# Kernel tuning notes

Hardware: AMD Instinct MI355X
Metric: run time of the kernel (lower is better)

The kernel has to match this reference:

```python
import jax, jax.numpy as jnp
import numpy as np

V, SMAX, D, L, H, F = 50257, 1024, 768, 12, 12, 3072
DH = D // H
SCALE = float(np.sqrt(DH))


def setup_inputs() -> dict:
    key = jax.random.key(0)
    ks = jax.random.split(key, 24)
    B, S = 2, 1024
    std = 0.02
    inp = {
        'input_ids': jax.random.randint(ks[0], (B, S), 0, V),
        'tok_emb': jax.random.normal(ks[1], (V, D), jnp.float32) * std,
        'pos_emb': jax.random.normal(ks[2], (SMAX, D), jnp.float32) * std,
        # stacked per-layer params (leading dim L)
        'Wq': jax.random.normal(ks[3], (L, D, D), jnp.float32) * std,
        'bq': jnp.zeros((L, D), jnp.float32),
        'Wk': jax.random.normal(ks[4], (L, D, D), jnp.float32) * std,
        'bk': jnp.zeros((L, D), jnp.float32),
        'Wv': jax.random.normal(ks[5], (L, D, D), jnp.float32) * std,
        'bv': jnp.zeros((L, D), jnp.float32),
        'Wo': jax.random.normal(ks[6], (L, D, D), jnp.float32) * std,
        'bo': jnp.zeros((L, D), jnp.float32),
        'ln1_g': jnp.ones((L, D), jnp.float32),
        'ln1_b': jnp.zeros((L, D), jnp.float32),
        'ln2_g': jnp.ones((L, D), jnp.float32),
        'ln2_b': jnp.zeros((L, D), jnp.float32),
        'W1': jax.random.normal(ks[7], (L, D, F), jnp.float32) * std,
        'b1': jnp.zeros((L, F), jnp.float32),
        'W2': jax.random.normal(ks[8], (L, F, D), jnp.float32) * std,
        'b2': jnp.zeros((L, D), jnp.float32),
        'lnf_g': jnp.ones((D,), jnp.float32),
        'lnf_b': jnp.zeros((D,), jnp.float32),
        'Whead': jax.random.normal(ks[9], (D, V), jnp.float32) * std,
    }
    return inp


def _layernorm(x, g, b, eps=1e-5):
    mu = jnp.mean(x, axis=-1, keepdims=True)
    var = jnp.var(x, axis=-1, keepdims=True)
    return (x - mu) * jax.lax.rsqrt(var + eps) * g + b


def _gpt_forward(input_ids, tok_emb, pos_emb, Wq, bq, Wk, bk, Wv, bv, Wo, bo,
                 ln1_g, ln1_b, ln2_g, ln2_b, W1, b1, W2, b2, lnf_g, lnf_b, Whead):
    B, S = input_ids.shape
    x = tok_emb[input_ids] + pos_emb[:S][None, :, :]  # (B,S,D)
    # additive causal mask: -inf above the diagonal
    idx = jnp.arange(S)
    neg_inf = jnp.finfo(x.dtype).min
    mask = jnp.where(idx[None, :] > idx[:, None], neg_inf, 0.0).astype(x.dtype)  # (S,S)

    def block(x, p):
        (wq, bq_, wk, bk_, wv, bv_, wo, bo_, g1, b1_, g2, b2_, w1, bb1, w2, bb2) = p
        h = _layernorm(x, g1, b1_)
        q = (h @ wq + bq_).reshape(B, S, H, DH)
        k = (h @ wk + bk_).reshape(B, S, H, DH)
        v = (h @ wv + bv_).reshape(B, S, H, DH)
        scores = jnp.einsum('bqhd,bkhd->bhqk', q, k) / SCALE + mask
        attn = jax.nn.softmax(scores, axis=-1)
        o = jnp.einsum('bhqk,bkhd->bqhd', attn, v).reshape(B, S, D)
        x = x + (o @ wo + bo_)
        h2 = _layernorm(x, g2, b2_)
        ffn = jax.nn.gelu(h2 @ w1 + bb1, approximate=False) @ w2 + bb2
        return x + ffn, None

    params = (Wq, bq, Wk, bk, Wv, bv, Wo, bo, ln1_g, ln1_b, ln2_g, ln2_b, W1, b1, W2, b2)
    x, _ = jax.lax.scan(block, x, params)
    x = _layernorm(x, lnf_g, lnf_b)
    return x @ Whead  # (B,S,V) logits


def reference(input_ids, tok_emb, pos_emb, Wq, bq, Wk, bk, Wv, bv, Wo, bo,
              ln1_g, ln1_b, ln2_g, ln2_b, W1, b1, W2, b2, lnf_g, lnf_b, Whead):
    return _gpt_forward(input_ids, tok_emb, pos_emb, Wq, bq, Wk, bk, Wv, bv, Wo, bo,
                        ln1_g, ln1_b, ln2_g, ln2_b, W1, b1, W2, b2, lnf_g, lnf_b, Whead)
```

## Files before the change

### kernel.cpp

```cpp
#include <hip/hip_runtime.h>
#include <hip/hip_bf16.h>
#include <cstdint>
#include <cstddef>

#define DEV __device__ __forceinline__

typedef __attribute__((ext_vector_type(8))) short short8;
typedef __attribute__((ext_vector_type(4))) short s16x4;
typedef __attribute__((ext_vector_type(4))) float f32x4;
typedef unsigned short u16;
typedef unsigned int u32;

static constexpr int Vv = 50257;
static constexpr int Dd = 768;
static constexpr int Ll = 12;
static constexpr int Hh = 12;
static constexpr int Ff = 3072;
static constexpr int Ss = 1024;
static constexpr int Bbatch = 2;
static constexpr int DHh = 64;
static constexpr int Mtok = Bbatch * Ss;
static constexpr int NQKV = 3 * Dd;
static constexpr int VPAD = 50304;

DEV u16 f2bf(float f){ u32 x; __builtin_memcpy(&x, &f, 4); x += 0x7fffu + ((x >> 16) & 1u); return (u16)(x >> 16); }

DEV void gld_lds16(const void* g, void* l){
  __builtin_amdgcn_global_load_lds((const __attribute__((address_space(1))) void*)g,
                                   (__attribute__((address_space(3))) void*)l, 16, 0, 0);
}

template<int N> DEV void waitv(){
  if constexpr (N == 0) asm volatile("s_waitcnt vmcnt(0)" ::: "memory");
  else if constexpr (N == 2) asm volatile("s_waitcnt vmcnt(2)" ::: "memory");
  else if constexpr (N == 3) asm volatile("s_waitcnt vmcnt(3)" ::: "memory");
  else if constexpr (N == 4) asm volatile("s_waitcnt vmcnt(4)" ::: "memory");
}
DEV void barrier_sb(){
  __builtin_amdgcn_s_barrier();
  __builtin_amdgcn_sched_barrier(0);
}

__global__ void k_embed(const int* __restrict__ ids, const float* __restrict__ tok,
                        const float* __restrict__ pos, float* __restrict__ x){
  int t = blockIdx.x;
  int id = ids[t];
  int s = t & (Ss - 1);
  const float* tr = tok + (size_t)id * Dd;
  const float* pr = pos + (size_t)s * Dd;
  float* xr = x + (size_t)t * Dd;
  for (int c = threadIdx.x; c < Dd; c += blockDim.x) xr[c] = tr[c] + pr[c];
}

__global__ __launch_bounds__(256) void k_ln(const float* __restrict__ x, const float* __restrict__ g,
                                            const float* __restrict__ b, u16* __restrict__ y){
  int row = blockIdx.x, tid = threadIdx.x;
  const float* xr = x + (size_t)row * Dd;
  float v0 = xr[tid], v1 = xr[tid + 256], v2 = xr[tid + 512];
  float s = v0 + v1 + v2, ss = v0 * v0 + v1 * v1 + v2 * v2;
  for (int o = 1; o < 64; o <<= 1){ s += __shfl_xor(s, o, 64); ss += __shfl_xor(ss, o, 64); }
  __shared__ float red[8];
  int w = tid >> 6, l = tid & 63;
  if (l == 0){ red[w] = s; red[w + 4] = ss; }
  __syncthreads();
  s = red[0] + red[1] + red[2] + red[3];
  ss = red[4] + red[5] + red[6] + red[7];
  float mu = s * (1.0f / Dd);
  float var = ss * (1.0f / Dd) - mu * mu;
  float rs = rsqrtf(var + 1e-5f);
  u16* yr = y + (size_t)row * Dd;
  yr[tid]       = f2bf((v0 - mu) * rs * g[tid]       + b[tid]);
  yr[tid + 256] = f2bf((v1 - mu) * rs * g[tid + 256] + b[tid + 256]);
  yr[tid + 512] = f2bf((v2 - mu) * rs * g[tid + 512] + b[tid + 512]);
}

__global__ __launch_bounds__(256) void k_transpose(const float* __restrict__ src, u16* __restrict__ dst,
                                                   int R, int C, long smat, long dmat){
  __shared__ float tile[64][33];
  src += (size_t)blockIdx.z * smat;
  dst += (size_t)blockIdx.z * dmat;
  int c0 = blockIdx.x * 32, r0 = blockIdx.y * 64;
  int tid = threadIdx.x;
  int tc = tid & 31, tr = tid >> 5;
  #pragma unroll
  for (int i = 0; i < 8; i++){
    int r = tr + i * 8, c = c0 + tc;
    tile[r][tc] = (c < C) ? src[(size_t)(r0 + r) * C + c] : 0.0f;
  }
  __syncthreads();
  #pragma unroll
  for (int it = 0; it < 2; it++){
    int id = it * 256 + tid;
    int c = id & 31, rg = id >> 5, r = rg * 4;
    int cc = c0 + c;
    if (cc < C){
      s16x4 v = { (short)f2bf(tile[r][c]), (short)f2bf(tile[r + 1][c]),
                  (short)f2bf(tile[r + 2][c]), (short)f2bf(tile[r + 3][c]) };
      *(s16x4*)(dst + (size_t)cc * R + r0 + r) = v;
    }
  }
}

__global__ void k_biaspack(const float* __restrict__ bq, const float* __restrict__ bk,
                           const float* __restrict__ bv, float* __restrict__ o){
  int i = blockIdx.x * 256 + threadIdx.x;
  int col = i % NQKV, lay = i / NQKV;
  float v = (col < Dd) ? bq[lay * Dd + col]
          : (col < 2 * Dd) ? bk[lay * Dd + col - Dd]
          : bv[lay * Dd + col - 2 * Dd];
  o[i] = v;
}

__global__ __launch_bounds__(256) void k_combine(const float* __restrict__ p,
                                                 const float* __restrict__ bias,
                                                 float* __restrict__ x){
  int i = blockIdx.x * 256 + threadIdx.x;
  constexpr size_t SL = (size_t)Mtok * Dd;
  f32x4 a  = ((const f32x4*)x)[i];
  f32x4 q0 = ((const f32x4*)p)[i];
  f32x4 q1 = ((const f32x4*)(p + SL))[i];
  f32x4 q2 = ((const f32x4*)(p + 2 * SL))[i];
  f32x4 q3 = ((const f32x4*)(p + 3 * SL))[i];
  int col0 = (i * 4) % Dd;
  f32x4 bv = *(const f32x4*)(bias + col0);
  ((f32x4*)x)[i] = a + (q0 + q1) + (q2 + q3) + bv;
}

template<int BM, int BN, int STRIDE, int EPI>
__global__ __launch_bounds__(256) void k_gemm3(const u16* __restrict__ A, const u16* __restrict__ Bt,
    const float* __restrict__ bias, float* __restrict__ Cf, u16* __restrict__ Cb,
    u16* __restrict__ vt, int Nn, int MT, int NT){
  constexpr int HM = BM / 2, HN = BN / 2, FM = HM / 16, FN = HN / 16;
  constexpr int nA = (BM * 4) / 256, nB = (BN * 4) / 256, NL = nA + nB;
  constexpr int ABUF = BM * 32, BBUF = BN * 32;
  __shared__ __align__(16) u16 ldsA[3 * ABUF];
  __shared__ __align__(16) u16 ldsB[3 * BBUF];
  int tid = threadIdx.x, wid = tid >> 6, l = tid & 63;
  int wm = wid >> 1, wn = wid & 1;
  int lr = l & 15, lc = l >> 4;
  int nwg = gridDim.x, dIdx = blockIdx.x;
  int L = (dIdx & 7) * (nwg >> 3) + (dIdx >> 3);
  int kidx = 0;
  if (EPI == 4){ int per = MT * NT; kidx = L / per; L -= kidx * per; }
  int mtile = L % MT, ntile = L / MT;
  int m0 = mtile * BM, n0 = ntile * BN;
  int kbase = kidx * 768;

  const u16* gA[nA]; u16* dA[nA];
  const u16* gB[nB]; u16* dB[nB];
  #pragma unroll
  for (int i = 0; i < nA; i++){
    int id = i * 256 + tid, row = id >> 2, c = id & 3;
    int cs = c ^ ((row >> 1) & 3);
    gA[i] = A + (size_t)(m0 + row) * STRIDE + kbase + cs * 8;
    dA[i] = ldsA + id * 8;
  }
  #pragma unroll
  for (int i = 0; i < nB; i++){
    int id = i * 256 + tid, row = id >> 2, c = id & 3;
    int cs = c ^ ((row >> 1) & 3);
    gB[i] = Bt + (size_t)(n0 + row) * STRIDE + kbase + cs * 8;
    dB[i] = ldsB + id * 8;
  }
  int offA[FM], offB[FN];
  #pragma unroll
  for (int i = 0; i < FM; i++){
    int row = wm * HM + i * 16 + lr;
    offA[i] = row * 64 + ((lc ^ ((row >> 1) & 3)) << 4);
  }
  #pragma unroll
  for (int j = 0; j < FN; j++){
    int row = wn * HN + j * 16 + lr;
    offB[j] = row * 64 + ((lc ^ ((row >> 1) & 3)) << 4);
  }

  f32x4 acc[FM][FN];
  #pragma unroll
  for (int i = 0; i < FM; i++)
    #pragma unroll
    for (int j = 0; j < FN; j++) acc[i][j] = (f32x4)0.0f;

  auto stage = [&](int buf){
    #pragma unroll
    for (int i = 0; i < nA; i++){ gld_lds16(gA[i], dA[i] + buf * ABUF); gA[i] += 32; }
    #pragma unroll
    for (int i = 0; i < nB; i++){ gld_lds16(gB[i], dB[i] + buf * BBUF); gB[i] += 32; }
  };
  auto compute = [&](int buf){
    const char* bA = (const char*)(ldsA + buf * ABUF);
    const char* bB = (const char*)(ldsB + buf * BBUF);
    short8 af[FM], bfr[FN];
    #pragma unroll
    for (int i = 0; i < FM; i++) af[i] = *(const short8*)(bA + offA[i]);
    #pragma unroll
    for (int j = 0; j < FN; j++) bfr[j] = *(const short8*)(bB + offB[j]);
    __builtin_amdgcn_s_setprio(1);
    #pragma unroll
    for (int i = 0; i < FM; i++)
      #pragma unroll
      for (int j = 0; j < FN; j++)
        acc[i][j] = __builtin_amdgcn_mfma_f32_16x16x32_bf16(af[i], bfr[j], acc[i][j], 0, 0, 0);
    __builtin_amdgcn_s_setprio(0);
  };

  stage(0); stage(1);
  waitv<NL>(); barrier_sb();
  #pragma unroll 1
  for (int tt = 0; tt < 21; tt += 3){
    stage(2); compute(0); waitv<NL>(); barrier_sb();
    stage(0); compute(1); waitv<NL>(); barrier_sb();
    stage(1); compute(2); waitv<NL>(); barrier_sb();
  }
  stage(2); compute(0); waitv<NL>(); barrier_sb();
  compute(1); waitv<0>(); barrier_sb();
  compute(2);

  if (EPI == 4){
    float* P = Cf + (size_t)kidx * Mtok * Dd;
    #pragma unroll
    for (int i = 0; i < FM; i++)
      #pragma unroll
      for (int j = 0; j < FN; j++){
        int col = n0 + wn * HN + j * 16 + lr;
        #pragma unroll
        for (int r = 0; r < 4; r++){
          int row = m0 + wm * HM + i * 16 + lc * 4 + r;
          P[(size_t)row * Dd + col] = acc[i][j][r];
        }
      }
    return;
  }
  #pragma unroll
  for (int i = 0; i < FM; i++){
    #pragma unroll
    for (int j = 0; j < FN; j++){
      int col = n0 + wn * HN + j * 16 + lr;
      if (EPI == 0 && col >= Nn) continue;
      float bv = (EPI == 1 || EPI == 2 || EPI == 3) ? bias[col] : 0.0f;
      u16 q4[4];
      #pragma unroll
      for (int r = 0; r < 4; r++){
        int row = m0 + wm * HM + i * 16 + lc * 4 + r;
        float v = acc[i][j][r] + bv;
        if (EPI == 1){ if (col < Dd) v *= 0.125f; }
        if (EPI == 2) v = 0.5f * v * (1.0f + erff(v * 0.70710678118f));
        if (EPI == 0){
          Cf[(size_t)row * Nn + col] = v;
        } else if (EPI == 3){
          Cf[(size_t)row * Nn + col] += v;
        } else {
          u16 bvv = f2bf(v);
          q4[r] = bvv;
          Cb[(size_t)row * Nn + col] = bvv;
        }
      }
      if (EPI == 1 && col >= 2 * Dd){
        int c2 = col - 2 * Dd, hh = c2 >> 6, dd2 = c2 & 63;
        int rowb = m0 + wm * HM + i * 16 + lc * 4;
        int bb = rowb >> 10, ss2 = rowb & 1023;
        s16x4 v4 = { (short)q4[0], (short)q4[1], (short)q4[2], (short)q4[3] };
        *(s16x4*)(vt + (((size_t)((bb * Hh + hh) * DHh + dd2)) << 10) + ss2) = v4;
      }
    }
  }
}

__global__ __launch_bounds__(256) void k_attn(const u16* __restrict__ qkv, const u16* __restrict__ vt,
                                              u16* __restrict__ o){
  constexpr int KB = 64 * 64;
  __shared__ __align__(16) u16 ldsK[3 * KB];
  __shared__ __align__(16) u16 ldsV[3 * KB];
  __shared__ __align__(16) u16 ldsP[4][16 * 72];
  int iq = blockIdx.x, bh = blockIdx.y, b = bh / Hh, h = bh % Hh;
  int tid = threadIdx.x, wid = tid >> 6, l = tid & 63, lr = l & 15, lc = l >> 4;
  int nt = iq + 1;
  int qrow = b * Ss + iq * 64 + wid * 16 + lr;
  const u16* qp = qkv + (size_t)qrow * NQKV + h * DHh;
  short8 qf0 = *(const short8*)(qp + lc * 8);
  short8 qf1 = *(const short8*)(qp + 32 + lc * 8);

  const u16* gK[2]; const u16* gV[2]; u16* dK[2]; u16* dV[2];
  #pragma unroll
  for (int c = 0; c < 2; c++){
    int id = c * 256 + tid, row = id >> 3, ch = id & 7;
    int cs = ch ^ (row & 7);
    gK[c] = qkv + (size_t)(b * Ss + row) * NQKV + Dd + h * DHh + cs * 8;
    gV[c] = vt + ((size_t)(bh * DHh) + row) * Ss + cs * 8;
    dK[c] = ldsK + id * 8;
    dV[c] = ldsV + id * 8;
  }
  auto stage = [&](int soff){
    #pragma unroll
    for (int c = 0; c < 2; c++){ gld_lds16(gK[c], dK[c] + soff); gK[c] += (size_t)64 * NQKV; }
    #pragma unroll
    for (int c = 0; c < 2; c++){ gld_lds16(gV[c], dV[c] + soff); gV[c] += 64; }
  };
  int koff[4][2], voff[4][2];
  #pragma unroll
  for (int fn = 0; fn < 4; fn++){
    int kv = fn * 16 + lr;
    #pragma unroll
    for (int ks = 0; ks < 2; ks++){
      int ch = ks * 4 + lc;
      koff[fn][ks] = kv * 128 + ((ch ^ (kv & 7)) << 4);
      voff[fn][ks] = koff[fn][ks];
    }
  }

  float mreg[4], lsum[4];
  f32x4 oacc[4];
  #pragma unroll
  for (int r = 0; r < 4; r++){ mreg[r] = -1e30f; lsum[r] = 0.0f; }
  #pragma unroll
  for (int i = 0; i < 4; i++) oacc[i] = (f32x4)0.0f;
  u16* pbase = ldsP[wid];

  if (nt > 1){ stage(0); stage(KB); waitv<4>(); }
  else       { stage(0); waitv<0>(); }
  barrier_sb();

  int cb = 0;
  #pragma unroll 1
  for (int t = 0; t < nt; ++t){
    int sb = (cb >= KB) ? (cb - KB) : (cb + 2 * KB);
    if (t + 2 < nt) stage(sb);
    const char* kbse = (const char*)ldsK + cb * 2;
    const char* vbse = (const char*)ldsV + cb * 2;
    f32x4 sc[4];
    #pragma unroll
    for (int fn = 0; fn < 4; fn++) sc[fn] = (f32x4)0.0f;
    #pragma unroll
    for (int fn = 0; fn < 4; fn++){
      short8 kf0 = *(const short8*)(kbse + koff[fn][0]);
      short8 kf1 = *(const short8*)(kbse + koff[fn][1]);
      sc[fn] = __builtin_amdgcn_mfma_f32_16x16x32_bf16(qf0, kf0, sc[fn], 0, 0, 0);
      sc[fn] = __builtin_amdgcn_mfma_f32_16x16x32_bf16(qf1, kf1, sc[fn], 0, 0, 0);
    }
    if (t == iq){
      #pragma unroll
      for (int fn = 0; fn < 4; fn++){
        int kv = fn * 16 + lr;
        #pragma unroll
        for (int r = 0; r < 4; r++){
          int qr = wid * 16 + lc * 4 + r;
          if (kv > qr) sc[fn][r] = -1e30f;
        }
      }
    }
    float alpha[4];
    #pragma unroll
    for (int r = 0; r < 4; r++){
      float mx = fmaxf(fmaxf(sc[0][r], sc[1][r]), fmaxf(sc[2][r], sc[3][r]));
      mx = fmaxf(mx, __shfl_xor(mx, 1, 64));
      mx = fmaxf(mx, __shfl_xor(mx, 2, 64));
      mx = fmaxf(mx, __shfl_xor(mx, 4, 64));
      mx = fmaxf(mx, __shfl_xor(mx, 8, 64));
      float mnew = fmaxf(mreg[r], mx);
      alpha[r] = __expf(mreg[r] - mnew);
      mreg[r] = mnew;
      float rsum = 0.0f;
      #pragma unroll
      for (int fn = 0; fn < 4; fn++){
        float p = __expf(sc[fn][r] - mnew);
        sc[fn][r] = p;
        rsum += p;
      }
      rsum += __shfl_xor(rsum, 1, 64);
      rsum += __shfl_xor(rsum, 2, 64);
      rsum += __shfl_xor(rsum, 4, 64);
      rsum += __shfl_xor(rsum, 8, 64);
      lsum[r] = lsum[r] * alpha[r] + rsum;
    }
    #pragma unroll
    for (int fn = 0; fn < 4; fn++)
      #pragma unroll
      for (int r = 0; r < 4; r++)
        pbase[(lc * 4 + r) * 72 + fn * 16 + lr] = f2bf(sc[fn][r]);
    asm volatile("s_waitcnt lgkmcnt(0)" ::: "memory");
    __builtin_amdgcn_sched_barrier(0);
    #pragma unroll
    for (int fd = 0; fd < 4; fd++)
      #pragma unroll
      for (int r = 0; r < 4; r++) oacc[fd][r] *= alpha[r];
    short8 pa0 = *(const short8*)((const char*)pbase + lr * 144 + lc * 16);
    short8 pa1 = *(const short8*)((const char*)pbase + lr * 144 + (4 + lc) * 16);
    #pragma unroll
    for (int fd = 0; fd < 4; fd++){
      short8 vf0 = *(const short8*)(vbse + voff[fd][0]);
      short8 vf1 = *(const short8*)(vbse + voff[fd][1]);
      oacc[fd] = __builtin_amdgcn_mfma_f32_16x16x32_bf16(pa0, vf0, oacc[fd], 0, 0, 0);
      oacc[fd] = __builtin_amdgcn_mfma_f32_16x16x32_bf16(pa1, vf1, oacc[fd], 0, 0, 0);
    }
    if (t + 2 < nt) waitv<4>(); else waitv<0>();
    barrier_sb();
    cb = (cb == 2 * KB) ? 0 : (cb + KB);
  }
  #pragma unroll
  for (int fd = 0; fd < 4; fd++)
    #pragma unroll
    for (int r = 0; r < 4; r++){
      int row = b * Ss + iq * 64 + wid * 16 + lc * 4 + r;
      o[(size_t)row * Dd + h * DHh + fd * 16 + lr] = f2bf(oacc[fd][r] / lsum[r]);
    }
}

extern "C" void kernel_launch(void* const* d_in, const int* in_sizes, int n_in,
                              void* d_out, int out_size, void* d_ws, size_t ws_size,
                              hipStream_t stream){
  const int*   ids  = (const int*)d_in[0];
  const float* tok  = (const float*)d_in[1];
  const float* pos  = (const float*)d_in[2];
  const float* Wq   = (const float*)d_in[3];
  const float* bq   = (const float*)d_in[4];
  const float* Wk   = (const float*)d_in[5];
  const float* bk   = (const float*)d_in[6];
  const float* Wv   = (const float*)d_in[7];
  const float* bv   = (const float*)d_in[8];
  const float* Wo   = (const float*)d_in[9];
  const float* bo   = (const float*)d_in[10];
  const float* ln1g = (const float*)d_in[11];
  const float* ln1b = (const float*)d_in[12];
  const float* ln2g = (const float*)d_in[13];
  const float* ln2b = (const float*)d_in[14];
  const float* W1   = (const float*)d_in[15];
  const float* b1   = (const float*)d_in[16];
  const float* W2   = (const float*)d_in[17];
  const float* b2   = (const float*)d_in[18];
  const float* lnfg = (const float*)d_in[19];
  const float* lnfb = (const float*)d_in[20];
  const float* Wh   = (const float*)d_in[21];
  float* out = (float*)d_out;

  auto al = [](size_t x){ return (x + 255) & ~(size_t)255; };
  size_t off = 0;
  auto take = [&](size_t bytes){ size_t r = off; off = al(off + bytes); return r; };
  size_t o_x    = take((size_t)Mtok * Dd * 4);
  size_t o_h    = take((size_t)Mtok * Dd * 2);
  size_t o_qkv  = take((size_t)Mtok * NQKV * 2);
  size_t o_vt   = take((size_t)Bbatch * Hh * DHh * Ss * 2);
  size_t o_o    = take((size_t)Mtok * Dd * 2);
  size_t o_mid  = take((size_t)Mtok * Ff * 2);
  size_t o_bq   = take((size_t)Ll * NQKV * 4);
  size_t o_part = take((size_t)4 * Mtok * Dd * 4);
  size_t o_rot = off;
  size_t o_wqkv, o_wo, o_w1, o_w2, o_wh;
  bool full;
  {
    size_t t = off;
    o_wqkv = t; t = al(t + (size_t)Ll * NQKV * Dd * 2);
    o_wo   = t; t = al(t + (size_t)Ll * Dd * Dd * 2);
    o_w1   = t; t = al(t + (size_t)Ll * Ff * Dd * 2);
    o_w2   = t; t = al(t + (size_t)Ll * Dd * Ff * 2);
    o_wh   = t; t = al(t + (size_t)VPAD * Dd * 2);
    full = (t <= ws_size);
  }
  char* ws = (char*)d_ws;
  float* x    = (float*)(ws + o_x);
  u16*   h    = (u16*)(ws + o_h);
  u16*   qkvb = (u16*)(ws + o_qkv);
  u16*   vtb  = (u16*)(ws + o_vt);
  u16*   ob   = (u16*)(ws + o_o);
  u16*   midb = (u16*)(ws + o_mid);
  float* bqkvp= (float*)(ws + o_bq);
  float* part = (float*)(ws + o_part);
  u16* wqkvT = full ? (u16*)(ws + o_wqkv) : (u16*)(ws + o_rot);
  u16* woT   = full ? (u16*)(ws + o_wo)   : (u16*)(ws + o_rot);
  u16* w1T   = full ? (u16*)(ws + o_w1)   : (u16*)(ws + o_rot);
  u16* w2T   = full ? (u16*)(ws + o_w2)   : (u16*)(ws + o_rot);
  u16* whT   = full ? (u16*)(ws + o_wh)   : (u16*)(ws + o_rot);

  auto tpose = [&](const float* src, u16* dst, int R, int C, int nmat, long smat, long dmat){
    k_transpose<<<dim3((C + 31) / 32, R / 64, nmat), 256, 0, stream>>>(src, dst, R, C, smat, dmat);
  };

  k_biaspack<<<(Ll * NQKV) / 256, 256, 0, stream>>>(bq, bk, bv, bqkvp);
  k_embed<<<Mtok, 256, 0, stream>>>(ids, tok, pos, x);

  if (full){
    tpose(Wq, wqkvT,              Dd, Dd, Ll, (long)Dd * Dd, (long)NQKV * Dd);
    tpose(Wk, wqkvT + Dd * Dd,    Dd, Dd, Ll, (long)Dd * Dd, (long)NQKV * Dd);
    tpose(Wv, wqkvT + 2 * Dd * Dd,Dd, Dd, Ll, (long)Dd * Dd, (long)NQKV * Dd);
    tpose(Wo, woT, Dd, Dd, Ll, (long)Dd * Dd, (long)Dd * Dd);
    tpose(W1, w1T, Dd, Ff, Ll, (long)Dd * Ff, (long)Ff * Dd);
    tpose(W2, w2T, Ff, Dd, Ll, (long)Ff * Dd, (long)Dd * Ff);
    tpose(Wh, whT, Dd, Vv, 1, 0, 0);
  }

  auto gemm_qkv = [&](const u16* Aop, const u16* Bop, const float* bias, u16* Cb){
    constexpr int MT = Mtok / 64, NT = NQKV / 128;
    k_gemm3<64, 128, Dd, 1><<<MT * NT, 256, 0, stream>>>(Aop, Bop, bias, nullptr, Cb, vtb, NQKV, MT, NT);
  };
  auto gemm_wo = [&](const u16* Aop, const u16* Bop, const float* bias, float* C){
    constexpr int MT = Mtok / 64, NT = Dd / 64;
    k_gemm3<64, 64, Dd, 3><<<MT * NT, 256, 0, stream>>>(Aop, Bop, bias, C, nullptr, nullptr, Dd, MT, NT);
  };
  auto gemm_ffn1 = [&](const u16* Aop, const u16* Bop, const float* bias, u16* Cb){
    constexpr int MT = Mtok / 64, NT = Ff / 128;
    k_gemm3<64, 128, Dd, 2><<<MT * NT, 256, 0, stream>>>(Aop, Bop, bias, nullptr, Cb, nullptr, Ff, MT, NT);
  };
  auto gemm_ffn2 = [&](const u16* Aop, const u16* Bop){
    constexpr int MT = Mtok / 128, NT = Dd / 128;
    k_gemm3<128, 128, Ff, 4><<<MT * NT * 4, 256, 0, stream>>>(Aop, Bop, nullptr, part, nullptr, nullptr, Dd, MT, NT);
  };
  auto gemm_head = [&](const u16* Aop, const u16* Bop, float* C){
    constexpr int MT = Mtok / 128, NT = VPAD / 128;
    k_gemm3<128, 128, Dd, 0><<<MT * NT, 256, 0, stream>>>(Aop, Bop, nullptr, C, nullptr, nullptr, Vv, MT, NT);
  };

  for (int l = 0; l < Ll; ++l){
    const u16* wqkvL = full ? wqkvT + (size_t)l * NQKV * Dd : wqkvT;
    const u16* woL   = full ? woT   + (size_t)l * Dd * Dd   : woT;
    const u16* w1L   = full ? w1T   + (size_t)l * Ff * Dd   : w1T;
    const u16* w2L   = full ? w2T   + (size_t)l * Dd * Ff   : w2T;
    if (!full){
      tpose(Wq + (size_t)l * Dd * Dd, wqkvT,              Dd, Dd, 1, 0, 0);
      tpose(Wk + (size_t)l * Dd * Dd, wqkvT + Dd * Dd,    Dd, Dd, 1, 0, 0);
      tpose(Wv + (size_t)l * Dd * Dd, wqkvT + 2 * Dd * Dd,Dd, Dd, 1, 0, 0);
    }
    k_ln<<<Mtok, 256, 0, stream>>>(x, ln1g + l * Dd, ln1b + l * Dd, h);
    gemm_qkv(h, wqkvL, bqkvp + l * NQKV, qkvb);
    k_attn<<<dim3(Ss / 64, Bbatch * Hh), 256, 0, stream>>>(qkvb, vtb, ob);
    if (!full) tpose(Wo + (size_t)l * Dd * Dd, woT, Dd, Dd, 1, 0, 0);
    gemm_wo(ob, woL, bo + l * Dd, x);
    k_ln<<<Mtok, 256, 0, stream>>>(x, ln2g + l * Dd, ln2b + l * Dd, h);
    if (!full) tpose(W1 + (size_t)l * Dd * Ff, w1T, Dd, Ff, 1, 0, 0);
    gemm_ffn1(h, w1L, b1 + l * Ff, midb);
    if (!full) tpose(W2 + (size_t)l * Ff * Dd, w2T, Ff, Dd, 1, 0, 0);
    gemm_ffn2(midb, w2L);
    k_combine<<<(Mtok * Dd / 4) / 256, 256, 0, stream>>>(part, b2 + l * Dd, x);
  }
  k_ln<<<Mtok, 256, 0, stream>>>(x, lnfg, lnfb, h);
  if (!full) tpose(Wh, whT, Dd, Vv, 1, 0, 0);
  gemm_head(h, whT, out);
}
```

Baseline: 2.308 ms.

## Fuse layernorms into embed/combine, rework GEMM and attention kernels

```diff
diff --git a/kernel.cpp b/kernel.cpp
--- a/kernel.cpp
+++ b/kernel.cpp
@@ -30,26 +30,33 @@
                                    (__attribute__((address_space(3))) void*)l, 16, 0, 0);
 }
 
-template<int N> DEV void waitv(){
-  if constexpr (N == 0) asm volatile("s_waitcnt vmcnt(0)" ::: "memory");
-  else if constexpr (N == 2) asm volatile("s_waitcnt vmcnt(2)" ::: "memory");
-  else if constexpr (N == 3) asm volatile("s_waitcnt vmcnt(3)" ::: "memory");
-  else if constexpr (N == 4) asm volatile("s_waitcnt vmcnt(4)" ::: "memory");
-}
-DEV void barrier_sb(){
-  __builtin_amdgcn_s_barrier();
-  __builtin_amdgcn_sched_barrier(0);
-}
-
-__global__ void k_embed(const int* __restrict__ ids, const float* __restrict__ tok,
-                        const float* __restrict__ pos, float* __restrict__ x){
-  int t = blockIdx.x;
+__global__ __launch_bounds__(256) void k_embed_ln(const int* __restrict__ ids, const float* __restrict__ tok,
+                                                  const float* __restrict__ pos, const float* __restrict__ g,
+                                                  const float* __restrict__ b, float* __restrict__ x,
+                                                  u16* __restrict__ h){
+  int t = blockIdx.x, tid = threadIdx.x;
   int id = ids[t];
   int s = t & (Ss - 1);
   const float* tr = tok + (size_t)id * Dd;
   const float* pr = pos + (size_t)s * Dd;
+  float v0 = tr[tid] + pr[tid], v1 = tr[tid + 256] + pr[tid + 256], v2 = tr[tid + 512] + pr[tid + 512];
   float* xr = x + (size_t)t * Dd;
-  for (int c = threadIdx.x; c < Dd; c += blockDim.x) xr[c] = tr[c] + pr[c];
+  xr[tid] = v0; xr[tid + 256] = v1; xr[tid + 512] = v2;
+  float sm = v0 + v1 + v2, ss = v0 * v0 + v1 * v1 + v2 * v2;
+  for (int o = 1; o < 64; o <<= 1){ sm += __shfl_xor(sm, o, 64); ss += __shfl_xor(ss, o, 64); }
+  __shared__ float red[8];
+  int w = tid >> 6, l = tid & 63;
+  if (l == 0){ red[w] = sm; red[w + 4] = ss; }
+  __syncthreads();
+  sm = red[0] + red[1] + red[2] + red[3];
+  ss = red[4] + red[5] + red[6] + red[7];
+  float mu = sm * (1.0f / Dd);
+  float var = ss * (1.0f / Dd) - mu * mu;
+  float rs = rsqrtf(var + 1e-5f);
+  u16* yr = h + (size_t)t * Dd;
+  yr[tid]       = f2bf((v0 - mu) * rs * g[tid]       + b[tid]);
+  yr[tid + 256] = f2bf((v1 - mu) * rs * g[tid + 256] + b[tid + 256]);
+  yr[tid + 512] = f2bf((v2 - mu) * rs * g[tid + 512] + b[tid + 512]);
 }
 
 __global__ __launch_bounds__(256) void k_ln(const float* __restrict__ x, const float* __restrict__ g,
@@ -74,6 +81,35 @@
   yr[tid + 512] = f2bf((v2 - mu) * rs * g[tid + 512] + b[tid + 512]);
 }
 
+__global__ __launch_bounds__(256) void k_combineln(const float* __restrict__ p, const float* __restrict__ bias,
+                                                   float* __restrict__ x, const float* __restrict__ g,
+                                                   const float* __restrict__ b, u16* __restrict__ h){
+  constexpr size_t SL = (size_t)Mtok * Dd;
+  int row = blockIdx.x, tid = threadIdx.x;
+  float* xr = x + (size_t)row * Dd;
+  const float* p0 = p + (size_t)row * Dd;
+  const float* p1 = p0 + SL;
+  float v0 = xr[tid]       + p0[tid]       + p1[tid]       + bias[tid];
+  float v1 = xr[tid + 256] + p0[tid + 256] + p1[tid + 256] + bias[tid + 256];
+  float v2 = xr[tid + 512] + p0[tid + 512] + p1[tid + 512] + bias[tid + 512];
+  xr[tid] = v0; xr[tid + 256] = v1; xr[tid + 512] = v2;
+  float s = v0 + v1 + v2, ss = v0 * v0 + v1 * v1 + v2 * v2;
+  for (int o = 1; o < 64; o <<= 1){ s += __shfl_xor(s, o, 64); ss += __shfl_xor(ss, o, 64); }
+  __shared__ float red[8];
+  int w = tid >> 6, l = tid & 63;
+  if (l == 0){ red[w] = s; red[w + 4] = ss; }
+  __syncthreads();
+  s = red[0] + red[1] + red[2] + red[3];
+  ss = red[4] + red[5] + red[6] + red[7];
+  float mu = s * (1.0f / Dd);
+  float var = ss * (1.0f / Dd) - mu * mu;
+  float rs = rsqrtf(var + 1e-5f);
+  u16* yr = h + (size_t)row * Dd;
+  yr[tid]       = f2bf((v0 - mu) * rs * g[tid]       + b[tid]);
+  yr[tid + 256] = f2bf((v1 - mu) * rs * g[tid + 256] + b[tid + 256]);
+  yr[tid + 512] = f2bf((v2 - mu) * rs * g[tid + 512] + b[tid + 512]);
+}
+
 __global__ __launch_bounds__(256) void k_transpose(const float* __restrict__ src, u16* __restrict__ dst,
                                                    int R, int C, long smat, long dmat){
   __shared__ float tile[64][33];
@@ -111,40 +147,29 @@
   o[i] = v;
 }
 
-__global__ __launch_bounds__(256) void k_combine(const float* __restrict__ p,
-                                                 const float* __restrict__ bias,
-                                                 float* __restrict__ x){
-  int i = blockIdx.x * 256 + threadIdx.x;
-  constexpr size_t SL = (size_t)Mtok * Dd;
-  f32x4 a  = ((const f32x4*)x)[i];
-  f32x4 q0 = ((const f32x4*)p)[i];
-  f32x4 q1 = ((const f32x4*)(p + SL))[i];
-  f32x4 q2 = ((const f32x4*)(p + 2 * SL))[i];
-  f32x4 q3 = ((const f32x4*)(p + 3 * SL))[i];
-  int col0 = (i * 4) % Dd;
-  f32x4 bv = *(const f32x4*)(bias + col0);
-  ((f32x4*)x)[i] = a + (q0 + q1) + (q2 + q3) + bv;
-}
-
-template<int BM, int BN, int STRIDE, int EPI>
-__global__ __launch_bounds__(256) void k_gemm3(const u16* __restrict__ A, const u16* __restrict__ Bt,
+template<int BM, int BN, int EPI>
+__global__ __launch_bounds__(256) void k_gemmF(const u16* __restrict__ A, const u16* __restrict__ Bt,
     const float* __restrict__ bias, float* __restrict__ Cf, u16* __restrict__ Cb,
     u16* __restrict__ vt, int Nn, int MT, int NT){
+  constexpr bool SPLIT = (EPI == 4);
+  constexpr int KST  = SPLIT ? Ff : Dd;
+  constexpr int KLEN = SPLIT ? (Ff / 2) : Dd;
+  constexpr int nk = KLEN / 32;
   constexpr int HM = BM / 2, HN = BN / 2, FM = HM / 16, FN = HN / 16;
-  constexpr int nA = (BM * 4) / 256, nB = (BN * 4) / 256, NL = nA + nB;
-  constexpr int ABUF = BM * 32, BBUF = BN * 32;
-  __shared__ __align__(16) u16 ldsA[3 * ABUF];
-  __shared__ __align__(16) u16 ldsB[3 * BBUF];
+  constexpr int nA = (BM * 4) / 256, nB = (BN * 4) / 256;
+  constexpr int ABYTE = BM * 64, BBYTE = BN * 64;
+  __shared__ __align__(16) u16 ldsA[2 * BM * 32];
+  __shared__ __align__(16) u16 ldsB[2 * BN * 32];
   int tid = threadIdx.x, wid = tid >> 6, l = tid & 63;
   int wm = wid >> 1, wn = wid & 1;
   int lr = l & 15, lc = l >> 4;
   int nwg = gridDim.x, dIdx = blockIdx.x;
   int L = (dIdx & 7) * (nwg >> 3) + (dIdx >> 3);
   int kidx = 0;
-  if (EPI == 4){ int per = MT * NT; kidx = L / per; L -= kidx * per; }
+  if (SPLIT){ int per = MT * NT; kidx = L / per; L -= kidx * per; }
   int mtile = L % MT, ntile = L / MT;
   int m0 = mtile * BM, n0 = ntile * BN;
-  int kbase = kidx * 768;
+  int kbase = kidx * KLEN;
 
   const u16* gA[nA]; u16* dA[nA];
   const u16* gB[nB]; u16* dB[nB];
@@ -152,14 +177,14 @@
   for (int i = 0; i < nA; i++){
     int id = i * 256 + tid, row = id >> 2, c = id & 3;
     int cs = c ^ ((row >> 1) & 3);
-    gA[i] = A + (size_t)(m0 + row) * STRIDE + kbase + cs * 8;
+    gA[i] = A + (size_t)(m0 + row) * KST + kbase + cs * 8;
     dA[i] = ldsA + id * 8;
   }
   #pragma unroll
   for (int i = 0; i < nB; i++){
     int id = i * 256 + tid, row = id >> 2, c = id & 3;
     int cs = c ^ ((row >> 1) & 3);
-    gB[i] = Bt + (size_t)(n0 + row) * STRIDE + kbase + cs * 8;
+    gB[i] = Bt + (size_t)(n0 + row) * KST + kbase + cs * 8;
     dB[i] = ldsB + id * 8;
   }
   int offA[FM], offB[FN];
@@ -182,84 +207,90 @@
 
   auto stage = [&](int buf){
     #pragma unroll
-    for (int i = 0; i < nA; i++){ gld_lds16(gA[i], dA[i] + buf * ABUF); gA[i] += 32; }
-    #pragma unroll
-    for (int i = 0; i < nB; i++){ gld_lds16(gB[i], dB[i] + buf * BBUF); gB[i] += 32; }
+    for (int i = 0; i < nA; i++){ gld_lds16(gA[i], (char*)dA[i] + buf * ABYTE); gA[i] += 32; }
+    #pragma unroll
+    for (int i = 0; i < nB; i++){ gld_lds16(gB[i], (char*)dB[i] + buf * BBYTE); gB[i] += 32; }
   };
   auto compute = [&](int buf){
-    const char* bA = (const char*)(ldsA + buf * ABUF);
-    const char* bB = (const char*)(ldsB + buf * BBUF);
+    const char* bA = (const char*)ldsA + buf * ABYTE;
+    const char* bB = (const char*)ldsB + buf * BBYTE;
     short8 af[FM], bfr[FN];
     #pragma unroll
     for (int i = 0; i < FM; i++) af[i] = *(const short8*)(bA + offA[i]);
     #pragma unroll
     for (int j = 0; j < FN; j++) bfr[j] = *(const short8*)(bB + offB[j]);
-    __builtin_amdgcn_s_setprio(1);
-    #pragma unroll
-    for (int i = 0; i < FM; i++)
-      #pragma unroll
-      for (int j = 0; j < FN; j++)
-        acc[i][j] = __builtin_amdgcn_mfma_f32_16x16x32_bf16(af[i], bfr[j], acc[i][j], 0, 0, 0);
-    __builtin_amdgcn_s_setprio(0);
-  };
-
-  stage(0); stage(1);
-  waitv<NL>(); barrier_sb();
-  #pragma unroll 1
-  for (int tt = 0; tt < 21; tt += 3){
-    stage(2); compute(0); waitv<NL>(); barrier_sb();
-    stage(0); compute(1); waitv<NL>(); barrier_sb();
-    stage(1); compute(2); waitv<NL>(); barrier_sb();
-  }
-  stage(2); compute(0); waitv<NL>(); barrier_sb();
-  compute(1); waitv<0>(); barrier_sb();
-  compute(2);
-
-  if (EPI == 4){
-    float* P = Cf + (size_t)kidx * Mtok * Dd;
     #pragma unroll
     for (int i = 0; i < FM; i++)
       #pragma unroll
       for (int j = 0; j < FN; j++){
+        if (EPI == 0)
+          acc[i][j] = __builtin_amdgcn_mfma_f32_16x16x32_bf16(af[i], bfr[j], acc[i][j], 0, 0, 0);
+        else
+          acc[i][j] = __builtin_amdgcn_mfma_f32_16x16x32_bf16(bfr[j], af[i], acc[i][j], 0, 0, 0);
+      }
+  };
+
+  stage(0);
+  __syncthreads();
+  #pragma unroll 1
+  for (int t = 0; t < nk - 1; ++t){
+    stage((t + 1) & 1);
+    compute(t & 1);
+    __syncthreads();
+  }
+  compute((nk - 1) & 1);
+
+  if (EPI == 0){
+    #pragma unroll
+    for (int i = 0; i < FM; i++){
+      #pragma unroll
+      for (int j = 0; j < FN; j++){
         int col = n0 + wn * HN + j * 16 + lr;
+        if (col >= Nn) continue;
         #pragma unroll
         for (int r = 0; r < 4; r++){
           int row = m0 + wm * HM + i * 16 + lc * 4 + r;
-          P[(size_t)row * Dd + col] = acc[i][j][r];
+          Cf[(size_t)row * Nn + col] = acc[i][j][r];
         }
       }
+    }
     return;
   }
   #pragma unroll
   for (int i = 0; i < FM; i++){
+    int row = m0 + wm * HM + i * 16 + lr;
     #pragma unroll
     for (int j = 0; j < FN; j++){
-      int col = n0 + wn * HN + j * 16 + lr;
-      if (EPI == 0 && col >= Nn) continue;
-      float bv = (EPI == 1 || EPI == 2 || EPI == 3) ? bias[col] : 0.0f;
-      u16 q4[4];
-      #pragma unroll
-      for (int r = 0; r < 4; r++){
-        int row = m0 + wm * HM + i * 16 + lc * 4 + r;
-        float v = acc[i][j][r] + bv;
-        if (EPI == 1){ if (col < Dd) v *= 0.125f; }
-        if (EPI == 2) v = 0.5f * v * (1.0f + erff(v * 0.70710678118f));
-        if (EPI == 0){
-          Cf[(size_t)row * Nn + col] = v;
-        } else if (EPI == 3){
-          Cf[(size_t)row * Nn + col] += v;
-        } else {
-          u16 bvv = f2bf(v);
-          q4[r] = bvv;
-          Cb[(size_t)row * Nn + col] = bvv;
-        }
-      }
-      if (EPI == 1 && col >= 2 * Dd){
-        int c2 = col - 2 * Dd, hh = c2 >> 6, dd2 = c2 & 63;
-        int rowb = m0 + wm * HM + i * 16 + lc * 4;
-        int bb = rowb >> 10, ss2 = rowb & 1023;
-        s16x4 v4 = { (short)q4[0], (short)q4[1], (short)q4[2], (short)q4[3] };
-        *(s16x4*)(vt + (((size_t)((bb * Hh + hh) * DHh + dd2)) << 10) + ss2) = v4;
+      int c0 = n0 + wn * HN + j * 16 + lc * 4;
+      f32x4 v = acc[i][j];
+      if (EPI == 4){
+        *(f32x4*)(Cf + (size_t)kidx * Mtok * Dd + (size_t)row * Dd + c0) = v;
+        continue;
+      }
+      f32x4 bv = *(const f32x4*)(bias + c0);
+      v = v + bv;
+      if (EPI == 3){
+        f32x4* p = (f32x4*)(Cf + (size_t)row * Nn + c0);
+        *p = *p + v;
+        continue;
+      }
+      if (EPI == 1 && c0 < Dd) v = v * 0.125f;
+      if (EPI == 2){
+        #pragma unroll
+        for (int r = 0; r < 4; r++) v[r] = 0.5f * v[r] * (1.0f + erff(v[r] * 0.70710678118f));
+      }
+      u16 q0 = f2bf(v[0]), q1 = f2bf(v[1]), q2 = f2bf(v[2]), q3 = f2bf(v[3]);
+      if (EPI == 1 && c0 >= 2 * Dd){
+        int c2 = c0 - 2 * Dd, hh = c2 >> 6, dd2 = c2 & 63;
+        int bb = row >> 10, ss2 = row & 1023;
+        size_t base = ((size_t)((bb * Hh + hh) * DHh + dd2)) << 10;
+        vt[base + ss2] = q0;
+        vt[base + (1 << 10) + ss2] = q1;
+        vt[base + (2 << 10) + ss2] = q2;
+        vt[base + (3 << 10) + ss2] = q3;
+      } else {
+        s16x4 pv = { (short)q0, (short)q1, (short)q2, (short)q3 };
+        *(s16x4*)(Cb + (size_t)row * Nn + c0) = pv;
       }
     }
   }
@@ -267,11 +298,13 @@
 
 __global__ __launch_bounds__(256) void k_attn(const u16* __restrict__ qkv, const u16* __restrict__ vt,
                                               u16* __restrict__ o){
-  constexpr int KB = 64 * 64;
-  __shared__ __align__(16) u16 ldsK[3 * KB];
-  __shared__ __align__(16) u16 ldsV[3 * KB];
+  __shared__ __align__(16) u16 ldsK[64 * 64];
+  __shared__ __align__(16) u16 ldsV[64 * 64];
   __shared__ __align__(16) u16 ldsP[4][16 * 72];
-  int iq = blockIdx.x, bh = blockIdx.y, b = bh / Hh, h = bh % Hh;
+  int bid = blockIdx.x;
+  int iq = (Ss / 64) - 1 - (bid / (Bbatch * Hh));
+  int bh = bid % (Bbatch * Hh);
+  int b = bh / Hh, h = bh % Hh;
   int tid = threadIdx.x, wid = tid >> 6, l = tid & 63, lr = l & 15, lc = l >> 4;
   int nt = iq + 1;
   int qrow = b * Ss + iq * 64 + wid * 16 + lr;
@@ -289,13 +322,7 @@
     dK[c] = ldsK + id * 8;
     dV[c] = ldsV + id * 8;
   }
-  auto stage = [&](int soff){
-    #pragma unroll
-    for (int c = 0; c < 2; c++){ gld_lds16(gK[c], dK[c] + soff); gK[c] += (size_t)64 * NQKV; }
-    #pragma unroll
-    for (int c = 0; c < 2; c++){ gld_lds16(gV[c], dV[c] + soff); gV[c] += 64; }
-  };
-  int koff[4][2], voff[4][2];
+  int koff[4][2];
   #pragma unroll
   for (int fn = 0; fn < 4; fn++){
     int kv = fn * 16 + lr;
@@ -303,105 +330,94 @@
     for (int ks = 0; ks < 2; ks++){
       int ch = ks * 4 + lc;
       koff[fn][ks] = kv * 128 + ((ch ^ (kv & 7)) << 4);
-      voff[fn][ks] = koff[fn][ks];
-    }
-  }
-
-  float mreg[4], lsum[4];
+    }
+  }
+
+  float mreg = -1e30f, lsum = 0.0f;
   f32x4 oacc[4];
-  #pragma unroll
-  for (int r = 0; r < 4; r++){ mreg[r] = -1e30f; lsum[r] = 0.0f; }
   #pragma unroll
   for (int i = 0; i < 4; i++) oacc[i] = (f32x4)0.0f;
   u16* pbase = ldsP[wid];
 
-  if (nt > 1){ stage(0); stage(KB); waitv<4>(); }
-  else       { stage(0); waitv<0>(); }
-  barrier_sb();
-
-  int cb = 0;
   #pragma unroll 1
   for (int t = 0; t < nt; ++t){
-    int sb = (cb >= KB) ? (cb - KB) : (cb + 2 * KB);
-    if (t + 2 < nt) stage(sb);
-    const char* kbse = (const char*)ldsK + cb * 2;
-    const char* vbse = (const char*)ldsV + cb * 2;
+    #pragma unroll
+    for (int c = 0; c < 2; c++){ gld_lds16(gK[c], dK[c]); gK[c] += (size_t)64 * NQKV; }
+    #pragma unroll
+    for (int c = 0; c < 2; c++){ gld_lds16(gV[c], dV[c]); gV[c] += 64; }
+    __syncthreads();
     f32x4 sc[4];
-    #pragma unroll
-    for (int fn = 0; fn < 4; fn++) sc[fn] = (f32x4)0.0f;
+    __builtin_amdgcn_s_setprio(1);
     #pragma unroll
     for (int fn = 0; fn < 4; fn++){
-      short8 kf0 = *(const short8*)(kbse + koff[fn][0]);
-      short8 kf1 = *(const short8*)(kbse + koff[fn][1]);
-      sc[fn] = __builtin_amdgcn_mfma_f32_16x16x32_bf16(qf0, kf0, sc[fn], 0, 0, 0);
-      sc[fn] = __builtin_amdgcn_mfma_f32_16x16x32_bf16(qf1, kf1, sc[fn], 0, 0, 0);
-    }
+      short8 kf0 = *(const short8*)((const char*)ldsK + koff[fn][0]);
+      short8 kf1 = *(const short8*)((const char*)ldsK + koff[fn][1]);
+      sc[fn] = __builtin_amdgcn_mfma_f32_16x16x32_bf16(kf0, qf0, (f32x4)0.0f, 0, 0, 0);
+      sc[fn] = __builtin_amdgcn_mfma_f32_16x16x32_bf16(kf1, qf1, sc[fn], 0, 0, 0);
+    }
+    __builtin_amdgcn_s_setprio(0);
     if (t == iq){
       #pragma unroll
-      for (int fn = 0; fn < 4; fn++){
-        int kv = fn * 16 + lr;
+      for (int fn = 0; fn < 4; fn++)
         #pragma unroll
-        for (int r = 0; r < 4; r++){
-          int qr = wid * 16 + lc * 4 + r;
-          if (kv > qr) sc[fn][r] = -1e30f;
-        }
-      }
-    }
-    float alpha[4];
-    #pragma unroll
-    for (int r = 0; r < 4; r++){
-      float mx = fmaxf(fmaxf(sc[0][r], sc[1][r]), fmaxf(sc[2][r], sc[3][r]));
-      mx = fmaxf(mx, __shfl_xor(mx, 1, 64));
-      mx = fmaxf(mx, __shfl_xor(mx, 2, 64));
-      mx = fmaxf(mx, __shfl_xor(mx, 4, 64));
-      mx = fmaxf(mx, __shfl_xor(mx, 8, 64));
-      float mnew = fmaxf(mreg[r], mx);
-      alpha[r] = __expf(mreg[r] - mnew);
-      mreg[r] = mnew;
-      float rsum = 0.0f;
+        for (int r = 0; r < 4; r++)
+          if (fn * 16 + lc * 4 + r > wid * 16 + lr) sc[fn][r] = -1e30f;
+    }
+    float pm = sc[0][0];
+    #pragma unroll
+    for (int fn = 0; fn < 4; fn++)
       #pragma unroll
-      for (int fn = 0; fn < 4; fn++){
+      for (int r = 0; r < 4; r++) pm = fmaxf(pm, sc[fn][r]);
+    pm = fmaxf(pm, __shfl_xor(pm, 16, 64));
+    pm = fmaxf(pm, __shfl_xor(pm, 32, 64));
+    float mnew = fmaxf(mreg, pm);
+    float alpha = __expf(mreg - mnew);
+    mreg = mnew;
+    float rs = 0.0f;
+    #pragma unroll
+    for (int fn = 0; fn < 4; fn++)
+      #pragma unroll
+      for (int r = 0; r < 4; r++){
         float p = __expf(sc[fn][r] - mnew);
         sc[fn][r] = p;
-        rsum += p;
-      }
-      rsum += __shfl_xor(rsum, 1, 64);
-      rsum += __shfl_xor(rsum, 2, 64);
-      rsum += __shfl_xor(rsum, 4, 64);
-      rsum += __shfl_xor(rsum, 8, 64);
-      lsum[r] = lsum[r] * alpha[r] + rsum;
-    }
-    #pragma unroll
-    for (int fn = 0; fn < 4; fn++)
-      #pragma unroll
-      for (int r = 0; r < 4; r++)
-        pbase[(lc * 4 + r) * 72 + fn * 16 + lr] = f2bf(sc[fn][r]);
+        rs += p;
+      }
+    rs += __shfl_xor(rs, 16, 64);
+    rs += __shfl_xor(rs, 32, 64);
+    lsum = lsum * alpha + rs;
+    #pragma unroll
+    for (int fn = 0; fn < 4; fn++){
+      s16x4 pv = { (short)f2bf(sc[fn][0]), (short)f2bf(sc[fn][1]),
+                   (short)f2bf(sc[fn][2]), (short)f2bf(sc[fn][3]) };
+      *(s16x4*)((char*)pbase + lr * 144 + fn * 32 + lc * 8) = pv;
+    }
     asm volatile("s_waitcnt lgkmcnt(0)" ::: "memory");
     __builtin_amdgcn_sched_barrier(0);
     #pragma unroll
     for (int fd = 0; fd < 4; fd++)
       #pragma unroll
-      for (int r = 0; r < 4; r++) oacc[fd][r] *= alpha[r];
+      for (int r = 0; r < 4; r++) oacc[fd][r] *= alpha;
     short8 pa0 = *(const short8*)((const char*)pbase + lr * 144 + lc * 16);
-    short8 pa1 = *(const short8*)((const char*)pbase + lr * 144 + (4 + lc) * 16);
+    short8 pa1 = *(const short8*)((const char*)pbase + lr * 144 + 64 + lc * 16);
+    __builtin_amdgcn_s_setprio(1);
     #pragma unroll
     for (int fd = 0; fd < 4; fd++){
-      short8 vf0 = *(const short8*)(vbse + voff[fd][0]);
-      short8 vf1 = *(const short8*)(vbse + voff[fd][1]);
-      oacc[fd] = __builtin_amdgcn_mfma_f32_16x16x32_bf16(pa0, vf0, oacc[fd], 0, 0, 0);
-      oacc[fd] = __builtin_amdgcn_mfma_f32_16x16x32_bf16(pa1, vf1, oacc[fd], 0, 0, 0);
-    }
-    if (t + 2 < nt) waitv<4>(); else waitv<0>();
-    barrier_sb();
-    cb = (cb == 2 * KB) ? 0 : (cb + KB);
-  }
-  #pragma unroll
-  for (int fd = 0; fd < 4; fd++)
-    #pragma unroll
-    for (int r = 0; r < 4; r++){
-      int row = b * Ss + iq * 64 + wid * 16 + lc * 4 + r;
-      o[(size_t)row * Dd + h * DHh + fd * 16 + lr] = f2bf(oacc[fd][r] / lsum[r]);
-    }
+      short8 vf0 = *(const short8*)((const char*)ldsV + koff[fd][0]);
+      short8 vf1 = *(const short8*)((const char*)ldsV + koff[fd][1]);
+      oacc[fd] = __builtin_amdgcn_mfma_f32_16x16x32_bf16(vf0, pa0, oacc[fd], 0, 0, 0);
+      oacc[fd] = __builtin_amdgcn_mfma_f32_16x16x32_bf16(vf1, pa1, oacc[fd], 0, 0, 0);
+    }
+    __builtin_amdgcn_s_setprio(0);
+    __syncthreads();
+  }
+  float inv = 1.0f / lsum;
+  int rowg = b * Ss + iq * 64 + wid * 16 + lr;
+  #pragma unroll
+  for (int fd = 0; fd < 4; fd++){
+    s16x4 ov = { (short)f2bf(oacc[fd][0] * inv), (short)f2bf(oacc[fd][1] * inv),
+                 (short)f2bf(oacc[fd][2] * inv), (short)f2bf(oacc[fd][3] * inv) };
+    *(s16x4*)(o + (size_t)rowg * Dd + h * DHh + fd * 16 + lc * 4) = ov;
+  }
 }
 
 extern "C" void kernel_launch(void* const* d_in, const int* in_sizes, int n_in,
@@ -441,7 +457,7 @@
   size_t o_o    = take((size_t)Mtok * Dd * 2);
   size_t o_mid  = take((size_t)Mtok * Ff * 2);
   size_t o_bq   = take((size_t)Ll * NQKV * 4);
-  size_t o_part = take((size_t)4 * Mtok * Dd * 4);
+  size_t o_part = take((size_t)2 * Mtok * Dd * 4);
   size_t o_rot = off;
   size_t o_wqkv, o_wo, o_w1, o_w2, o_wh;
   bool full;
@@ -474,7 +490,7 @@
   };
 
   k_biaspack<<<(Ll * NQKV) / 256, 256, 0, stream>>>(bq, bk, bv, bqkvp);
-  k_embed<<<Mtok, 256, 0, stream>>>(ids, tok, pos, x);
+  k_embed_ln<<<Mtok, 256, 0, stream>>>(ids, tok, pos, ln1g, ln1b, x, h);
 
   if (full){
     tpose(Wq, wqkvT,              Dd, Dd, Ll, (long)Dd * Dd, (long)NQKV * Dd);
@@ -488,23 +504,23 @@
 
   auto gemm_qkv = [&](const u16* Aop, const u16* Bop, const float* bias, u16* Cb){
     constexpr int MT = Mtok / 64, NT = NQKV / 128;
-    k_gemm3<64, 128, Dd, 1><<<MT * NT, 256, 0, stream>>>(Aop, Bop, bias, nullptr, Cb, vtb, NQKV, MT, NT);
+    k_gemmF<64, 128, 1><<<MT * NT, 256, 0, stream>>>(Aop, Bop, bias, nullptr, Cb, vtb, NQKV, MT, NT);
   };
   auto gemm_wo = [&](const u16* Aop, const u16* Bop, const float* bias, float* C){
     constexpr int MT = Mtok / 64, NT = Dd / 64;
-    k_gemm3<64, 64, Dd, 3><<<MT * NT, 256, 0, stream>>>(Aop, Bop, bias, C, nullptr, nullptr, Dd, MT, NT);
+    k_gemmF<64, 64, 3><<<MT * NT, 256, 0, stream>>>(Aop, Bop, bias, C, nullptr, nullptr, Dd, MT, NT);
   };
   auto gemm_ffn1 = [&](const u16* Aop, const u16* Bop, const float* bias, u16* Cb){
     constexpr int MT = Mtok / 64, NT = Ff / 128;
-    k_gemm3<64, 128, Dd, 2><<<MT * NT, 256, 0, stream>>>(Aop, Bop, bias, nullptr, Cb, nullptr, Ff, MT, NT);
+    k_gemmF<64, 128, 2><<<MT * NT, 256, 0, stream>>>(Aop, Bop, bias, nullptr, Cb, nullptr, Ff, MT, NT);
   };
   auto gemm_ffn2 = [&](const u16* Aop, const u16* Bop){
-    constexpr int MT = Mtok / 128, NT = Dd / 128;
-    k_gemm3<128, 128, Ff, 4><<<MT * NT * 4, 256, 0, stream>>>(Aop, Bop, nullptr, part, nullptr, nullptr, Dd, MT, NT);
+    constexpr int MT = Mtok / 64, NT = Dd / 64;
+    k_gemmF<64, 64, 4><<<MT * NT * 2, 256, 0, stream>>>(Aop, Bop, nullptr, part, nullptr, nullptr, Dd, MT, NT);
   };
   auto gemm_head = [&](const u16* Aop, const u16* Bop, float* C){
     constexpr int MT = Mtok / 128, NT = VPAD / 128;
-    k_gemm3<128, 128, Dd, 0><<<MT * NT, 256, 0, stream>>>(Aop, Bop, nullptr, C, nullptr, nullptr, Vv, MT, NT);
+    k_gemmF<128, 128, 0><<<MT * NT, 256, 0, stream>>>(Aop, Bop, nullptr, C, nullptr, nullptr, Vv, MT, NT);
   };
 
   for (int l = 0; l < Ll; ++l){
@@ -517,9 +533,8 @@
       tpose(Wk + (size_t)l * Dd * Dd, wqkvT + Dd * Dd,    Dd, Dd, 1, 0, 0);
       tpose(Wv + (size_t)l * Dd * Dd, wqkvT + 2 * Dd * Dd,Dd, Dd, 1, 0, 0);
     }
-    k_ln<<<Mtok, 256, 0, stream>>>(x, ln1g + l * Dd, ln1b + l * Dd, h);
     gemm_qkv(h, wqkvL, bqkvp + l * NQKV, qkvb);
-    k_attn<<<dim3(Ss / 64, Bbatch * Hh), 256, 0, stream>>>(qkvb, vtb, ob);
+    k_attn<<<(Ss / 64) * Bbatch * Hh, 256, 0, stream>>>(qkvb, vtb, ob);
     if (!full) tpose(Wo + (size_t)l * Dd * Dd, woT, Dd, Dd, 1, 0, 0);
     gemm_wo(ob, woL, bo + l * Dd, x);
     k_ln<<<Mtok, 256, 0, stream>>>(x, ln2g + l * Dd, ln2b + l * Dd, h);
@@ -527,9 +542,10 @@
     gemm_ffn1(h, w1L, b1 + l * Ff, midb);
     if (!full) tpose(W2 + (size_t)l * Ff * Dd, w2T, Ff, Dd, 1, 0, 0);
     gemm_ffn2(midb, w2L);
-    k_combine<<<(Mtok * Dd / 4) / 256, 256, 0, stream>>>(part, b2 + l * Dd, x);
-  }
-  k_ln<<<Mtok, 256, 0, stream>>>(x, lnfg, lnfb, h);
+    const float* gN = (l + 1 < Ll) ? (ln1g + (l + 1) * Dd) : lnfg;
+    const float* bN = (l + 1 < Ll) ? (ln1b + (l + 1) * Dd) : lnfb;
+    k_combineln<<<Mtok, 256, 0, stream>>>(part, b2 + l * Dd, x, gN, bN, h);
+  }
   if (!full) tpose(Wh, whT, Dd, Vv, 1, 0, 0);
   gemm_head(h, whT, out);
 }
```

Result: faster. 2.133 ms (-7.6%).
